# Kernel tuning notes

Hardware: AMD Instinct MI355X
Metric: run time of the kernel (lower is better)

## Reference

```python
import jax, jax.numpy as jnp
import numpy as np

E = 1024
H = 16
NUM_WEIGHTS = 9


def setup_inputs() -> dict:
    key = jax.random.key(0)
    ks = jax.random.split(key, 5)
    T, B = 1024, 4
    x = jax.random.normal(ks[0], (T, B, E), dtype=jnp.float32)
    # xavier-uniform-ish init scales
    w_in = jax.random.uniform(ks[1], (NUM_WEIGHTS * E, E), dtype=jnp.float32,
                              minval=-1.0, maxval=1.0) * np.sqrt(6.0 / (NUM_WEIGHTS * E + E))
    b_in = jnp.zeros((NUM_WEIGHTS * E,), dtype=jnp.float32)
    w_out = jax.random.uniform(ks[2], (E, E), dtype=jnp.float32,
                               minval=-1.0, maxval=1.0) * np.sqrt(6.0 / (E + E))
    b_out = jnp.zeros((E,), dtype=jnp.float32)
    return {"x": x, "w_in": w_in, "b_in": b_in, "w_out": w_out, "b_out": b_out}


def _heads(t, T, B, hd):
    # [T, B, E] -> [B*H, T, hd]
    return t.reshape(T, B * H, hd).transpose(1, 0, 2)


def reference(x, w_in, b_in, w_out, b_out):
    T, B, _ = x.shape
    hd = E // H
    scaling = hd ** -0.5
    gumbel_alpha = 1.0  # const_gumbel_alpha path

    proj = jnp.einsum('tbe,fe->tbf', x, w_in) + b_in  # [T, B, 9E]
    (q, k, v, q_left, k_left, q_right, k_right,
     q_local, k_local) = jnp.split(proj, NUM_WEIGHTS, axis=-1)

    q = q * scaling
    q_local = q_local * scaling

    q, k, v = _heads(q, T, B, hd), _heads(k, T, B, hd), _heads(v, T, B, hd)
    q_left, k_left = _heads(q_left, T, B, hd), _heads(k_left, T, B, hd)
    q_right, k_right = _heads(q_right, T, B, hd), _heads(k_right, T, B, hd)
    q_local, k_local = _heads(q_local, T, B, hd), _heads(k_local, T, B, hd)

    # --- prepare_local_masking (no padding mask) ---
    left_w = jnp.einsum('btd,bsd->bts', q_left, k_left)    # [BH, T, S]
    right_w = jnp.einsum('btd,bsd->bts', q_right, k_right)
    left_sm = jax.nn.softmax(gumbel_alpha * left_w, axis=-1)
    right_sm = jax.nn.softmax(gumbel_alpha * right_w, axis=-1)

    triu = jnp.triu(jnp.ones((T, T), dtype=x.dtype))       # [S, S]
    triu_t = triu.T
    # compute_lrmask2localmask
    left_mask = left_sm @ triu
    right_mask = right_sm @ triu_t
    bw_left_mask = left_sm @ triu_t
    bw_right_mask = right_sm @ triu
    local_mask = left_mask * right_mask + bw_left_mask * bw_right_mask  # [BH, T, S]

    # --- global attention branch ---
    global_w = jnp.einsum('btd,bsd->bts', q, k)
    global_probs = jax.nn.softmax(global_w, axis=-1)

    # --- local attention branch, gated by differentiable-window mask ---
    local_w = jnp.einsum('btd,bsd->bts', q_local, k_local)
    local_sm = jax.nn.softmax(local_w, axis=-1)
    masked_local = local_sm * local_mask
    local_probs = masked_local / masked_local.sum(axis=-1, keepdims=True)

    attn_probs = 0.5 * (global_probs + local_probs)
    attn = jnp.einsum('bts,bsd->btd', attn_probs, v)        # [BH, T, hd]
    attn = attn.transpose(1, 0, 2).reshape(T, B, E)
    out = jnp.einsum('tbe,fe->tbf', attn, w_out) + b_out
    return out
```

## Files before the change

kernel.cpp:

```cpp
#include <hip/hip_runtime.h>
#include <math.h>


typedef _Float16 half8 __attribute__((ext_vector_type(8)));
typedef _Float16 half4v __attribute__((ext_vector_type(4)));
typedef _Float16 half2v __attribute__((ext_vector_type(2)));
typedef float f32x4 __attribute__((ext_vector_type(4)));

#define MFMA16(A, B, C) __builtin_amdgcn_mfma_f32_16x16x32_f16(A, B, C, 0, 0, 0)

#define SMEM_ATTN ((1088 + 10240 + 256 * 65) * 4)

static __device__ __forceinline__ unsigned packhl(_Float16 a, _Float16 b) {
  half2v v; v[0] = a; v[1] = b;
  return __builtin_bit_cast(unsigned, v);
}

__global__ __launch_bounds__(256)
void split_hl(const float* __restrict__ x, _Float16* __restrict__ xh,
              _Float16* __restrict__ xl) {
  const int i = blockIdx.x * 256 + threadIdx.x;
  const float4 v = ((const float4*)x)[i];
  half4v h, l;
  const float* f = (const float*)&v;
#pragma unroll
  for (int e = 0; e < 4; ++e) {
    h[e] = (_Float16)f[e];
    l[e] = (_Float16)(f[e] - (float)h[e]);
  }
  ((half4v*)xh)[i] = h;
  ((half4v*)xl)[i] = l;
}

template<int MODE>
__global__ __launch_bounds__(256, 2)
void gemm_mfma(const float* __restrict__ A, const float* __restrict__ B,
               const float* __restrict__ bias, float* __restrict__ C,
               _Float16* __restrict__ Ph, _Float16* __restrict__ Pl,
               const _Float16* __restrict__ Axh, const _Float16* __restrict__ Axl,
               int M, int N, int K) {
  __shared__ _Float16 Ah[128 * 64], Al[128 * 64], Bh[128 * 64], Bl[128 * 64];
  const int tid = threadIdx.x;
  const int m0 = blockIdx.x * 128, n0 = blockIdx.y * 128;
  const int wave = tid >> 6, lane = tid & 63;
  const int g2 = lane >> 4, c = lane & 15;
  const int wm = (wave >> 1) * 64, wn = (wave & 1) * 64;

  const int srow = tid >> 1;
  const int shalf = (tid & 1) * 32;
  const int swz = (srow & 7) << 3;
  const float* ap = A + (size_t)(m0 + srow) * K + shalf;
  const float* bp = B + (size_t)(n0 + srow) * K + shalf;
  const _Float16* aph = Axh + (size_t)(m0 + srow) * K + shalf;
  const _Float16* apl = Axl + (size_t)(m0 + srow) * K + shalf;

  f32x4 acc[4][4];
#pragma unroll
  for (int i = 0; i < 4; ++i)
#pragma unroll
    for (int j = 0; j < 4; ++j) acc[i][j] = (f32x4){0.f, 0.f, 0.f, 0.f};

  for (int k0 = 0; k0 < K; k0 += 64) {
    float4 av[8], bv[8];
    half8 ah8[4], al8[4];
    if (MODE == 1) {
#pragma unroll
      for (int u = 0; u < 4; ++u) {
        ah8[u] = *(const half8*)(aph + k0 + u * 8);
        al8[u] = *(const half8*)(apl + k0 + u * 8);
      }
    } else {
#pragma unroll
      for (int u = 0; u < 8; ++u) av[u] = *(const float4*)(ap + k0 + u * 4);
    }
#pragma unroll
    for (int u = 0; u < 8; ++u) bv[u] = *(const float4*)(bp + k0 + u * 4);
    __syncthreads();
    if (MODE == 1) {
#pragma unroll
      for (int u = 0; u < 4; ++u) {
        const int cc = (shalf + u * 8) ^ swz;
        *(half8*)&Ah[srow * 64 + cc] = ah8[u];
        *(half8*)&Al[srow * 64 + cc] = al8[u];
      }
    }
#pragma unroll
    for (int u = 0; u < 8; ++u) {
      const int cc = (shalf + u * 4) ^ swz;
      half4v h4b, l4b;
      const float* fb = (const float*)&bv[u];
#pragma unroll
      for (int e = 0; e < 4; ++e) {
        _Float16 hb = (_Float16)fb[e];
        h4b[e] = hb; l4b[e] = (_Float16)(fb[e] - (float)hb);
      }
      if (MODE == 0) {
        half4v h4a, l4a;
        const float* fa = (const float*)&av[u];
#pragma unroll
        for (int e = 0; e < 4; ++e) {
          _Float16 ha = (_Float16)fa[e];
          h4a[e] = ha; l4a[e] = (_Float16)(fa[e] - (float)ha);
        }
        *(half4v*)&Ah[srow * 64 + cc] = h4a;
        *(half4v*)&Al[srow * 64 + cc] = l4a;
      }
      *(half4v*)&Bh[srow * 64 + cc] = h4b;
      *(half4v*)&Bl[srow * 64 + cc] = l4b;
    }
    __syncthreads();
#pragma unroll
    for (int ks = 0; ks < 2; ++ks) {
      const int kb = ks * 32 + 8 * g2;
      half8 a_h[4], a_l[4];
#pragma unroll
      for (int i = 0; i < 4; ++i) {
        const int row = wm + i * 16 + c;
        const int cc = kb ^ ((row & 7) << 3);
        a_h[i] = *(const half8*)&Ah[row * 64 + cc];
        a_l[i] = *(const half8*)&Al[row * 64 + cc];
      }
#pragma unroll
      for (int j = 0; j < 4; ++j) {
        const int rowb = wn + j * 16 + c;
        const int cc = kb ^ ((rowb & 7) << 3);
        const half8 b_h = *(const half8*)&Bh[rowb * 64 + cc];
        const half8 b_l = *(const half8*)&Bl[rowb * 64 + cc];
#pragma unroll
        for (int i = 0; i < 4; ++i) {
          acc[i][j] = MFMA16(a_h[i], b_h, acc[i][j]);
          acc[i][j] = MFMA16(a_h[i], b_l, acc[i][j]);
          acc[i][j] = MFMA16(a_l[i], b_h, acc[i][j]);
        }
      }
    }
  }

#pragma unroll
  for (int j = 0; j < 4; ++j) {
    const int nj = n0 + wn + j * 16 + c;
    const float bz = bias[nj];
    if (MODE == 0) {
#pragma unroll
      for (int i = 0; i < 4; ++i)
#pragma unroll
        for (int q = 0; q < 4; ++q) {
          const int mi = m0 + wm + i * 16 + 4 * g2 + q;
          C[(size_t)mi * N + nj] = acc[i][j][q] + bz;
        }
    } else {
      const int w = nj >> 10, hh = (nj >> 6) & 15, d = nj & 63;
      const float scale = (w == 0 || w == 7) ? 0.125f : 1.0f;
#pragma unroll
      for (int i = 0; i < 4; ++i)
#pragma unroll
        for (int q = 0; q < 4; ++q) {
          const int mi = m0 + wm + i * 16 + 4 * g2 + q;
          const int t = mi >> 2, b2 = mi & 3;
          const size_t bb = ((size_t)w * 64 + (b2 * 16 + hh)) * 65536;
          size_t idx;
          if (w == 2) {
            idx = bb + (size_t)(((t >> 6) * 2 + ((t >> 5) & 1)) * 4 + (d >> 4)) * 512
                     + ((t >> 3) & 3) * 128 + (d & 15) * 8 + (t & 7);
          } else {
            idx = bb + (size_t)t * 64 + d;
          }
          const float v = (acc[i][j][q] + bz) * scale;
          const _Float16 h16 = (_Float16)v;
          Ph[idx] = h16;
          Pl[idx] = (_Float16)(v - (float)h16);
        }
    }
  }
}

__global__ __launch_bounds__(1024, 4)
void attn_mfma(const _Float16* __restrict__ Ph, const _Float16* __restrict__ Pl,
               float* __restrict__ attnOut) {
  extern __shared__ float smem[];
  float* sRed = smem;
  _Float16* sChunk = (_Float16*)(smem + 1088);
  float* sOut = smem + 1088 + 10240;
  const int flat = blockIdx.x;
  const int nf = (flat & 7) * 512 + (flat >> 3);
  const int bh = nf >> 6;
  const int t0 = (nf & 63) << 4;
  const int tid = threadIdx.x;
  const int wave = tid >> 6, lane = tid & 63;
  const int g2 = lane >> 4, c = lane & 15;
  const int sbase = wave << 6;

  auto mbase = [&](int w) { return ((size_t)w * 64 + bh) * 65536; };

  struct QF { half8 h0, h1, l0, l1; };
  auto loadQ = [&](int wq) {
    QF f;
    const _Float16* qh = Ph + mbase(wq) + (size_t)(t0 + c) * 64 + 8 * g2;
    const _Float16* ql = Pl + mbase(wq) + (size_t)(t0 + c) * 64 + 8 * g2;
    f.h0 = *(const half8*)qh; f.h1 = *(const half8*)(qh + 32);
    f.l0 = *(const half8*)ql; f.l1 = *(const half8*)(ql + 32);
    return f;
  };
  auto stileT = [&](const QF& f, const _Float16* kbh, const _Float16* kbl, int tp) {
    const int s0 = sbase + tp * 16;
    const _Float16* kh = kbh + (size_t)(s0 + c) * 64 + 8 * g2;
    const _Float16* kl = kbl + (size_t)(s0 + c) * 64 + 8 * g2;
    const half8 ah0 = *(const half8*)kh, ah1 = *(const half8*)(kh + 32);
    const half8 al0 = *(const half8*)kl, al1 = *(const half8*)(kl + 32);
    f32x4 a = {0.f, 0.f, 0.f, 0.f};
    a = MFMA16(ah0, f.h0, a);
    a = MFMA16(ah1, f.h1, a);
    a = MFMA16(ah0, f.l0, a);
    a = MFMA16(ah1, f.l1, a);
    a = MFMA16(al0, f.h0, a);
    a = MFMA16(al1, f.h1, a);
    return a;
  };

  auto put = [&](int slot, float val) {
    if (lane < 16) sRed[slot * 272 + c * 17 + wave] = val;
  };
  auto sum_pref = [&](int slot, float& pref) {
    float S = 0.f;
    pref = 0.f;
    const float* p = sRed + slot * 272 + c * 17;
#pragma unroll
    for (int w = 0; w < 16; ++w) {
      const float t = p[w];
      S += t;
      if (w < wave) pref += t;
    }
    return S;
  };
  auto sum_only = [&](int slot) {
    float S = 0.f;
    const float* p = sRed + slot * 272 + c * 17;
#pragma unroll
    for (int w = 0; w < 16; ++w) S += p[w];
    return S;
  };
  auto scan_s = [&](f32x4* v) {
    float carry = 0.f;
#pragma unroll
    for (int m = 0; m < 4; ++m) {
      v[m][1] += v[m][0];
      v[m][2] += v[m][1];
      v[m][3] += v[m][2];
      const float B = v[m][3];
      float sc = B;
      const float u1 = __shfl_up(sc, 16, 64);
      if (g2 >= 1) sc += u1;
      const float u2 = __shfl_up(sc, 32, 64);
      if (g2 >= 2) sc += u2;
      const float e = sc - B + carry;
      v[m][0] += e; v[m][1] += e; v[m][2] += e; v[m][3] += e;
      carry += __shfl(sc, 48 + c, 64);
    }
    return carry;
  };
  auto rowsum = [&](const f32x4* v) {
    float s = 0.f;
#pragma unroll
    for (int m = 0; m < 4; ++m) s += (v[m][0] + v[m][1]) + (v[m][2] + v[m][3]);
    s += __shfl_xor(s, 16, 64);
    s += __shfl_xor(s, 32, 64);
    return s;
  };

  f32x4 lv[4], rv[4], ov[4], gv[4];

  {
    const QF fL = loadQ(3);
    const QF fR = loadQ(5);
    const _Float16* k4h = Ph + mbase(4);
    const _Float16* k4l = Pl + mbase(4);
    const _Float16* k6h = Ph + mbase(6);
    const _Float16* k6l = Pl + mbase(6);
#pragma unroll
    for (int m = 0; m < 4; ++m) {
      lv[m] = stileT(fL, k4h, k4l, m);
      rv[m] = stileT(fR, k6h, k6l, m);
    }
#pragma unroll
    for (int m = 0; m < 4; ++m)
#pragma unroll
      for (int q = 0; q < 4; ++q) {
        lv[m][q] = __expf(lv[m][q]);
        rv[m][q] = __expf(rv[m][q]);
      }
    put(0, scan_s(lv));
    put(1, scan_s(rv));
  }
  __syncthreads();
  {
    const QF fO = loadQ(7);
    const QF fG = loadQ(0);
    const _Float16* k8h = Ph + mbase(8);
    const _Float16* k8l = Pl + mbase(8);
    const _Float16* k1h = Ph + mbase(1);
    const _Float16* k1l = Pl + mbase(1);
#pragma unroll
    for (int m = 0; m < 4; ++m) {
      ov[m] = stileT(fO, k8h, k8l, m);
      gv[m] = stileT(fG, k1h, k1l, m);
    }
  }
  {
    float prefL, prefR;
    const float SL = sum_pref(0, prefL);
    const float SR = sum_pref(1, prefR);
    const float invSL = 1.f / SL, invSR = 1.f / SR;
#pragma unroll
    for (int m = 0; m < 4; ++m)
#pragma unroll
      for (int q = 0; q < 4; ++q) {
        lv[m][q] = (lv[m][q] + prefL) * invSL;
        rv[m][q] = (rv[m][q] + prefR) * invSR;
      }
    const float bL = prefL * invSL, bR = prefR * invSR;
#pragma unroll
    for (int m = 3; m >= 0; --m) {
      const float aU = __shfl_up(lv[m][3], 16, 64);
      const float bU = __shfl_up(rv[m][3], 16, 64);
      const float aM = (m > 0) ? __shfl(lv[m - 1][3], 48 + c, 64) : bL;
      const float bM = (m > 0) ? __shfl(rv[m - 1][3], 48 + c, 64) : bR;
      const float a0 = (g2 == 0) ? aM : aU;
      const float b0 = (g2 == 0) ? bM : bU;
      f32x4 nm;
      nm[0] = lv[m][0] * (1.f - b0)        + (1.f - a0)        * rv[m][0];
      nm[1] = lv[m][1] * (1.f - rv[m][0])  + (1.f - lv[m][0])  * rv[m][1];
      nm[2] = lv[m][2] * (1.f - rv[m][1])  + (1.f - lv[m][1])  * rv[m][2];
      nm[3] = lv[m][3] * (1.f - rv[m][2])  + (1.f - lv[m][2])  * rv[m][3];
      lv[m] = nm;
    }
  }
  {
#pragma unroll
    for (int m = 0; m < 4; ++m)
#pragma unroll
      for (int q = 0; q < 4; ++q) {
        ov[m][q] = __expf(ov[m][q]) * lv[m][q];
        gv[m][q] = __expf(gv[m][q]);
      }
    put(2, rowsum(ov));
    put(3, rowsum(gv));
  }
  __syncthreads();
  unsigned Hp[4][2], Lp[4][2];
  {
    const float scO = 0.5f / sum_only(2);
    const float scG = 0.5f / sum_only(3);
#pragma unroll
    for (int m = 0; m < 4; ++m)
#pragma unroll
      for (int p = 0; p < 2; ++p) {
        const float x0 = ov[m][2 * p] * scO + gv[m][2 * p] * scG;
        const float x1 = ov[m][2 * p + 1] * scO + gv[m][2 * p + 1] * scG;
        const _Float16 h0 = (_Float16)x0, h1 = (_Float16)x1;
        Hp[m][p] = packhl(h0, h1);
        Lp[m][p] = packhl((_Float16)(x0 - (float)h0), (_Float16)(x1 - (float)h1));
      }
  }
  f32x4 cacc[4];
#pragma unroll
  for (int dt = 0; dt < 4; ++dt) cacc[dt] = (f32x4){0.f, 0.f, 0.f, 0.f};
  {
    _Float16* chw = sChunk + wave * (2 * 16 * 40);
    const _Float16* vbh = Ph + mbase(2);
    const _Float16* vbl = Pl + mbase(2);
#pragma unroll
    for (int kk = 0; kk < 2; ++kk) {
#pragma unroll
      for (int mlo = 0; mlo < 2; ++mlo)
#pragma unroll
        for (int p = 0; p < 2; ++p) {
          const int off = c * 40 + 16 * mlo + 4 * g2 + 2 * p;
          *(unsigned*)&chw[off] = Hp[2 * kk + mlo][p];
          *(unsigned*)&chw[640 + off] = Lp[2 * kk + mlo][p];
        }
      const half8 pah = *(const half8*)&chw[c * 40 + 8 * g2];
      const half8 pal = *(const half8*)&chw[640 + c * 40 + 8 * g2];
#pragma unroll
      for (int dt = 0; dt < 4; ++dt) {
        const size_t vo = (size_t)(((wave * 2 + kk) * 4 + dt) << 9) + (g2 << 7) + (c << 3);
        const half8 bh8 = *(const half8*)(vbh + vo);
        const half8 bl8 = *(const half8*)(vbl + vo);
        cacc[dt] = MFMA16(pah, bh8, cacc[dt]);
        cacc[dt] = MFMA16(pah, bl8, cacc[dt]);
        cacc[dt] = MFMA16(pal, bh8, cacc[dt]);
      }
    }
  }
#pragma unroll
  for (int dt = 0; dt < 4; ++dt)
#pragma unroll
    for (int q = 0; q < 4; ++q)
      sOut[(wave * 16 + 4 * g2 + q) * 65 + dt * 16 + c] = cacc[dt][q];
  __syncthreads();
  {
    const int b2 = bh >> 4, hh = bh & 15;
    const int r = tid >> 6, d = tid & 63;
    float a = 0.f;
#pragma unroll
    for (int w = 0; w < 16; ++w) a += sOut[(w * 16 + r) * 65 + d];
    attnOut[((size_t)(t0 + r) * 4 + b2) * 1024 + hh * 64 + d] = a;
  }
}

extern "C" void kernel_launch(void* const* d_in, const int* in_sizes, int n_in,
                              void* d_out, int out_size, void* d_ws, size_t ws_size,
                              hipStream_t stream) {
  const float* x     = (const float*)d_in[0];
  const float* w_in  = (const float*)d_in[1];
  const float* b_in  = (const float*)d_in[2];
  const float* w_out = (const float*)d_in[3];
  const float* b_out = (const float*)d_in[4];

  const size_t NP = (size_t)9 * 64 * 1024 * 64;
  _Float16* Ph = (_Float16*)d_ws;
  _Float16* Pl = Ph + NP;
  float* attn = (float*)(Pl + NP);
  _Float16* xh = (_Float16*)attn;
  _Float16* xl = xh + (size_t)4096 * 1024;

  (void)hipFuncSetAttribute((const void*)attn_mfma,
                            hipFuncAttributeMaxDynamicSharedMemorySize,
                            SMEM_ATTN);

  split_hl<<<4096, 256, 0, stream>>>(x, xh, xl);
  gemm_mfma<1><<<dim3(32, 72), 256, 0, stream>>>(nullptr, w_in, b_in, nullptr, Ph, Pl, xh, xl, 4096, 9216, 1024);
  attn_mfma<<<4096, 1024, SMEM_ATTN, stream>>>(Ph, Pl, attn);
  gemm_mfma<0><<<dim3(32, 8), 256, 0, stream>>>(attn, w_out, b_out, (float*)d_out, nullptr, nullptr, nullptr, nullptr, 4096, 1024, 1024);
}
```

Before: 968.1 us.

## Cut register pressure in attn_mfma to double occupancy target

Raises the launch-bounds minimum blocks hint from 4 to 8 and restructures the score computation so fewer live register arrays exist at once. Each score branch is now computed and consumed in turn, and the accumulators are reused (ov/gv folded into lv/rv). K fragments are loaded one at a time right before their MFMAs. This trades latency hiding from batched independent loads and MFMAs for higher wave occupancy, and may force spills if the compiler cannot fit the tighter register budget.

```diff
diff --git a/kernel.cpp b/kernel.cpp
--- a/kernel.cpp
+++ b/kernel.cpp
@@ -174,7 +174,7 @@
   }
 }
 
-__global__ __launch_bounds__(1024, 4)
+__global__ __launch_bounds__(1024, 8)
 void attn_mfma(const _Float16* __restrict__ Ph, const _Float16* __restrict__ Pl,
                float* __restrict__ attnOut) {
   extern __shared__ float smem[];
@@ -205,15 +205,17 @@
     const int s0 = sbase + tp * 16;
     const _Float16* kh = kbh + (size_t)(s0 + c) * 64 + 8 * g2;
     const _Float16* kl = kbl + (size_t)(s0 + c) * 64 + 8 * g2;
-    const half8 ah0 = *(const half8*)kh, ah1 = *(const half8*)(kh + 32);
-    const half8 al0 = *(const half8*)kl, al1 = *(const half8*)(kl + 32);
     f32x4 a = {0.f, 0.f, 0.f, 0.f};
-    a = MFMA16(ah0, f.h0, a);
-    a = MFMA16(ah1, f.h1, a);
-    a = MFMA16(ah0, f.l0, a);
-    a = MFMA16(ah1, f.l1, a);
-    a = MFMA16(al0, f.h0, a);
-    a = MFMA16(al1, f.h1, a);
+    half8 t = *(const half8*)kh;
+    a = MFMA16(t, f.h0, a);
+    a = MFMA16(t, f.l0, a);
+    t = *(const half8*)(kh + 32);
+    a = MFMA16(t, f.h1, a);
+    a = MFMA16(t, f.l1, a);
+    t = *(const half8*)kl;
+    a = MFMA16(t, f.h0, a);
+    t = *(const half8*)(kl + 32);
+    a = MFMA16(t, f.h1, a);
     return a;
   };
 
@@ -267,44 +269,33 @@
     return s;
   };
 
-  f32x4 lv[4], rv[4], ov[4], gv[4];
+  f32x4 lv[4], rv[4];
 
   {
     const QF fL = loadQ(3);
-    const QF fR = loadQ(5);
     const _Float16* k4h = Ph + mbase(4);
     const _Float16* k4l = Pl + mbase(4);
+#pragma unroll
+    for (int m = 0; m < 4; ++m) {
+      lv[m] = stileT(fL, k4h, k4l, m);
+#pragma unroll
+      for (int q = 0; q < 4; ++q) lv[m][q] = __expf(lv[m][q]);
+    }
+    put(0, scan_s(lv));
+  }
+  {
+    const QF fR = loadQ(5);
     const _Float16* k6h = Ph + mbase(6);
     const _Float16* k6l = Pl + mbase(6);
 #pragma unroll
     for (int m = 0; m < 4; ++m) {
-      lv[m] = stileT(fL, k4h, k4l, m);
       rv[m] = stileT(fR, k6h, k6l, m);
-    }
-#pragma unroll
-    for (int m = 0; m < 4; ++m)
-#pragma unroll
-      for (int q = 0; q < 4; ++q) {
-        lv[m][q] = __expf(lv[m][q]);
-        rv[m][q] = __expf(rv[m][q]);
-      }
-    put(0, scan_s(lv));
+#pragma unroll
+      for (int q = 0; q < 4; ++q) rv[m][q] = __expf(rv[m][q]);
+    }
     put(1, scan_s(rv));
   }
   __syncthreads();
-  {
-    const QF fO = loadQ(7);
-    const QF fG = loadQ(0);
-    const _Float16* k8h = Ph + mbase(8);
-    const _Float16* k8l = Pl + mbase(8);
-    const _Float16* k1h = Ph + mbase(1);
-    const _Float16* k1l = Pl + mbase(1);
-#pragma unroll
-    for (int m = 0; m < 4; ++m) {
-      ov[m] = stileT(fO, k8h, k8l, m);
-      gv[m] = stileT(fG, k1h, k1l, m);
-    }
-  }
   {
     float prefL, prefR;
     const float SL = sum_pref(0, prefL);
@@ -335,15 +326,28 @@
     }
   }
   {
-#pragma unroll
-    for (int m = 0; m < 4; ++m)
-#pragma unroll
-      for (int q = 0; q < 4; ++q) {
-        ov[m][q] = __expf(ov[m][q]) * lv[m][q];
-        gv[m][q] = __expf(gv[m][q]);
-      }
-    put(2, rowsum(ov));
-    put(3, rowsum(gv));
+    const QF fO = loadQ(7);
+    const _Float16* k8h = Ph + mbase(8);
+    const _Float16* k8l = Pl + mbase(8);
+#pragma unroll
+    for (int m = 0; m < 4; ++m) {
+      const f32x4 x = stileT(fO, k8h, k8l, m);
+#pragma unroll
+      for (int q = 0; q < 4; ++q) lv[m][q] = __expf(x[q]) * lv[m][q];
+    }
+    put(2, rowsum(lv));
+  }
+  {
+    const QF fG = loadQ(0);
+    const _Float16* k1h = Ph + mbase(1);
+    const _Float16* k1l = Pl + mbase(1);
+#pragma unroll
+    for (int m = 0; m < 4; ++m) {
+      const f32x4 x = stileT(fG, k1h, k1l, m);
+#pragma unroll
+      for (int q = 0; q < 4; ++q) rv[m][q] = __expf(x[q]);
+    }
+    put(3, rowsum(rv));
   }
   __syncthreads();
   unsigned Hp[4][2], Lp[4][2];
@@ -354,8 +358,8 @@
     for (int m = 0; m < 4; ++m)
 #pragma unroll
       for (int p = 0; p < 2; ++p) {
-        const float x0 = ov[m][2 * p] * scO + gv[m][2 * p] * scG;
-        const float x1 = ov[m][2 * p + 1] * scO + gv[m][2 * p + 1] * scG;
+        const float x0 = lv[m][2 * p] * scO + rv[m][2 * p] * scG;
+        const float x1 = lv[m][2 * p + 1] * scO + rv[m][2 * p + 1] * scG;
         const _Float16 h0 = (_Float16)x0, h1 = (_Float16)x1;
         Hp[m][p] = packhl(h0, h1);
         Lp[m][p] = packhl((_Float16)(x0 - (float)h0), (_Float16)(x1 - (float)h1));
```

New measurement: 1.244 ms. 28.5% more time.
